# Kernel optimization log

Hardware: AMD Instinct MI355X
Metric: run time of the kernel (lower is better)

Reference implementation:

```python
import jax, jax.numpy as jnp
import numpy as np

L, N = 200, 256  # event_list_length, num_nodes


def setup_inputs() -> dict:
    key = jax.random.key(0)
    ks = jax.random.split(key, 7)
    time = jax.random.uniform(ks[0], (2,), dtype=jnp.float32)
    event_list = jax.random.normal(ks[1], (L + 1, N, N), dtype=jnp.float32)
    u_begin = jax.random.uniform(ks[2], (N, N, 3), dtype=jnp.float32)
    # xavier-ish scales for params
    a = jax.random.normal(ks[3], (L, N, N, 3), dtype=jnp.float32) * 0.05
    w = jax.random.normal(ks[4], (L, N, 1, N), dtype=jnp.float32) * 0.05
    liner_w = jax.random.normal(ks[5], (N, 3), dtype=jnp.float32) * 0.5
    liner_b = jax.random.normal(ks[6], (N,), dtype=jnp.float32) * 0.1
    return {"time": time, "event_list": event_list, "u_begin": u_begin,
            "a": a, "w": w, "liner_w": liner_w, "liner_b": liner_b,
            "batch_size": 2}


def reference(time, event_list, u_begin, a, w, liner_w, liner_b, batch_size):
    # event_list[:-1]; consumed in pairs (start, start+1) with batch_size == 2
    T = event_list.shape[0] - 1
    S = T // batch_size                      # number of scan steps
    n = event_list.shape[1]
    e2 = event_list[:T].reshape(S, 2, n, n)          # [S,2,N,N]
    a2 = a[:T].reshape(S, 2, n, n, 3)                # [S,2,N,N,3]
    w2 = w[:T, :, 0, :].reshape(S, 2, n, n)          # [S,2,N,N] (squeeze the 1-dim)
    t0, t1 = time[0], time[1]                        # original always uses time[0], time[1]

    def step(u, xs):
        ep, ap, wp = xs                              # [2,N,N], [2,N,N,3], [2,N,N]
        # per-node scalar dot: w[start][node] @ event_begin[k][node]
        dot0 = jnp.einsum('nk,nk->n', wp[0], ep[0])  # [N]
        dot1 = jnp.einsum('nk,nk->n', wp[1], ep[1])
        # math.exp in the original returns a Python float -> constant w.r.t. autograd
        f0 = jax.lax.stop_gradient(jnp.exp(-dot0 * t0))[:, None, None]
        f1 = jax.lax.stop_gradient(jnp.exp(-dot1 * t1))[:, None, None]
        lamda = u + ap[0] * f0 + ap[1] * f1          # [N,N,3]
        temp = jax.nn.softmax(lamda, axis=-1)        # softmax over the 3-dim (dim=1 of [N,3] per node)
        # per-node Linear(3,1): temp[node] @ W_node^T + b_node -> [N,N]
        out = jnp.einsum('nmc,nc->nm', temp, liner_w) + liner_b[:, None]
        # state update was .detach().cpu().numpy() -> stop_gradient
        return jax.lax.stop_gradient(temp), out

    _, outs = jax.lax.scan(step, u_begin, (e2, a2, w2))
    return outs                                      # [S, N, N] == [T/2, N, N]
```

## Files before the change

### kernel.cpp

```cpp
#include <hip/hip_runtime.h>


#define NN   256
#define TT   200
#define SS   100

__global__ __launch_bounds__(256) void fused_scan_kernel(
    const float* __restrict__ timep,
    const float* __restrict__ ev,
    const float* __restrict__ ub,
    const float* __restrict__ a,
    const float* __restrict__ w,
    const float* __restrict__ lw,
    const float* __restrict__ lb,
    float* __restrict__ out)
{
    __shared__ float fs[TT];

    const int n    = blockIdx.x;
    const int m    = threadIdx.x;
    const int lane = m & 63;
    const int wid  = m >> 6;

    const float t0 = timep[0];
    const float t1 = timep[1];
    const float tsel = (wid & 1) ? t1 : t0;

    {
        const size_t rowoff = (size_t)n * NN;
        for (int t = wid; t < TT; t += 8) {
            const int t2 = t + 4;
            const float4* wp0 = (const float4*)(w  + (size_t)t  * (NN * NN) + rowoff);
            const float4* ep0 = (const float4*)(ev + (size_t)t  * (NN * NN) + rowoff);
            const float4* wp1 = (const float4*)(w  + (size_t)t2 * (NN * NN) + rowoff);
            const float4* ep1 = (const float4*)(ev + (size_t)t2 * (NN * NN) + rowoff);
            float4 wv0 = wp0[lane];
            float4 ev0 = ep0[lane];
            float4 wv1 = wp1[lane];
            float4 ev1 = ep1[lane];
            float d0 = wv0.x * ev0.x;
            d0 = fmaf(wv0.y, ev0.y, d0);
            d0 = fmaf(wv0.z, ev0.z, d0);
            d0 = fmaf(wv0.w, ev0.w, d0);
            float d1 = wv1.x * ev1.x;
            d1 = fmaf(wv1.y, ev1.y, d1);
            d1 = fmaf(wv1.z, ev1.z, d1);
            d1 = fmaf(wv1.w, ev1.w, d1);
#pragma unroll
            for (int off = 1; off < 64; off <<= 1) {
                d0 += __shfl_xor(d0, off, 64);
                d1 += __shfl_xor(d1, off, 64);
            }
            if (lane == 0) {
                fs[t]  = __expf(-d0 * tsel);
                fs[t2] = __expf(-d1 * tsel);
            }
        }
    }
    __syncthreads();

    const size_t base    = (size_t)n * (NN * 3) + (size_t)m * 3;
    const size_t TSTRIDE = (size_t)NN * NN * 3;
    const float* ap = a + base;

    float u0 = ub[base + 0];
    float u1 = ub[base + 1];
    float u2 = ub[base + 2];

    const float w0 = lw[n * 3 + 0];
    const float w1 = lw[n * 3 + 1];
    const float w2 = lw[n * 3 + 2];
    const float bb = lb[n];

    float c0x = ap[0],            c0y = ap[1],            c0z = ap[2];
    float c1x = ap[TSTRIDE + 0],  c1y = ap[TSTRIDE + 1],  c1z = ap[TSTRIDE + 2];
    const float* ap1 = ap + 2 * TSTRIDE;
    float n0x = ap1[0],           n0y = ap1[1],           n0z = ap1[2];
    float n1x = ap1[TSTRIDE + 0], n1y = ap1[TSTRIDE + 1], n1z = ap1[TSTRIDE + 2];

    float* op = out + (size_t)n * NN + m;

    for (int s = 0; s < SS; ++s) {
        const int sp = (s + 2 < SS) ? (s + 2) : 0;
        const float* app = ap + (size_t)(2 * sp) * TSTRIDE;
        float p0x = app[0];
        float p0y = app[1];
        float p0z = app[2];
        float p1x = app[TSTRIDE + 0];
        float p1y = app[TSTRIDE + 1];
        float p1z = app[TSTRIDE + 2];

        const float f0 = fs[2 * s];
        const float f1 = fs[2 * s + 1];

        float l0 = fmaf(c0x, f0, fmaf(c1x, f1, u0));
        float l1 = fmaf(c0y, f0, fmaf(c1y, f1, u1));
        float l2 = fmaf(c0z, f0, fmaf(c1z, f1, u2));
        float mx = fmaxf(l0, fmaxf(l1, l2));
        float e0 = __expf(l0 - mx);
        float e1 = __expf(l1 - mx);
        float e2 = __expf(l2 - mx);
        float inv = __builtin_amdgcn_rcpf(e0 + e1 + e2);
        u0 = e0 * inv;
        u1 = e1 * inv;
        u2 = e2 * inv;
        op[(size_t)s * (NN * NN)] = fmaf(u0, w0, fmaf(u1, w1, fmaf(u2, w2, bb)));

        c0x = n0x; c0y = n0y; c0z = n0z;
        c1x = n1x; c1y = n1y; c1z = n1z;
        n0x = p0x; n0y = p0y; n0z = p0z;
        n1x = p1x; n1y = p1y; n1z = p1z;
    }
}

extern "C" void kernel_launch(void* const* d_in, const int* in_sizes, int n_in,
                              void* d_out, int out_size, void* d_ws, size_t ws_size,
                              hipStream_t stream) {
    const float* timep = (const float*)d_in[0];
    const float* ev    = (const float*)d_in[1];
    const float* ub    = (const float*)d_in[2];
    const float* a     = (const float*)d_in[3];
    const float* w     = (const float*)d_in[4];
    const float* lw    = (const float*)d_in[5];
    const float* lb    = (const float*)d_in[6];
    float* out = (float*)d_out;

    fused_scan_kernel<<<NN, 256, 0, stream>>>(timep, ev, ub, a, w, lw, lb, out);
}
```

Measured before the change: 305.1 us.

## Split exp-factor precompute into a wide kernel and deepen the a-prefetch pipeline

Moves the per-node dot-product and exp factor computation out of the 256-block scan kernel into its own kernel, which launches one wave per (t, n) pair and writes the results to workspace. The scan kernel then loads its 200 factors from workspace. Its prefetch of the `a` coefficients is also deepened from 2 steps ahead to 5 steps ahead, using a register ring buffer in an unrolled loop. The aim is to spread the ~100 MB of w/ev reads across many more blocks and hide more load latency in the serial scan. The cost is an extra launch, a workspace round trip, and higher register pressure.

```diff
diff --git a/kernel.cpp b/kernel.cpp
--- a/kernel.cpp
+++ b/kernel.cpp
@@ -1,62 +1,55 @@
 #include <hip/hip_runtime.h>
 
 
-#define NN   256
-#define TT   200
-#define SS   100
+#define NN 256
+#define TT 200
+#define SS 100
+#define DEPTH 5
 
-__global__ __launch_bounds__(256) void fused_scan_kernel(
+__global__ __launch_bounds__(256) void f_kernel(
     const float* __restrict__ timep,
     const float* __restrict__ ev,
+    const float* __restrict__ w,
+    float* __restrict__ fs)
+{
+    const int lane = threadIdx.x & 63;
+    const int gwave = blockIdx.x * 4 + (threadIdx.x >> 6);
+    const int t = gwave >> 8;
+    const int n = gwave & 255;
+
+    const size_t rowoff = (size_t)t * (NN * NN) + (size_t)n * NN;
+    const float4* wp = (const float4*)(w + rowoff);
+    const float4* ep = (const float4*)(ev + rowoff);
+    float4 wv = wp[lane];
+    float4 evv = ep[lane];
+    float d = wv.x * evv.x;
+    d = fmaf(wv.y, evv.y, d);
+    d = fmaf(wv.z, evv.z, d);
+    d = fmaf(wv.w, evv.w, d);
+#pragma unroll
+    for (int off = 1; off < 64; off <<= 1)
+        d += __shfl_xor(d, off, 64);
+
+    if (lane == 0) {
+        const float tsel = (t & 1) ? timep[1] : timep[0];
+        fs[n * TT + t] = __expf(-d * tsel);
+    }
+}
+
+__global__ __launch_bounds__(256) void scan_kernel(
+    const float* __restrict__ fs_g,
     const float* __restrict__ ub,
     const float* __restrict__ a,
-    const float* __restrict__ w,
     const float* __restrict__ lw,
     const float* __restrict__ lb,
     float* __restrict__ out)
 {
     __shared__ float fs[TT];
 
-    const int n    = blockIdx.x;
-    const int m    = threadIdx.x;
-    const int lane = m & 63;
-    const int wid  = m >> 6;
+    const int n = blockIdx.x;
+    const int m = threadIdx.x;
 
-    const float t0 = timep[0];
-    const float t1 = timep[1];
-    const float tsel = (wid & 1) ? t1 : t0;
-
-    {
-        const size_t rowoff = (size_t)n * NN;
-        for (int t = wid; t < TT; t += 8) {
-            const int t2 = t + 4;
-            const float4* wp0 = (const float4*)(w  + (size_t)t  * (NN * NN) + rowoff);
-            const float4* ep0 = (const float4*)(ev + (size_t)t  * (NN * NN) + rowoff);
-            const float4* wp1 = (const float4*)(w  + (size_t)t2 * (NN * NN) + rowoff);
-            const float4* ep1 = (const float4*)(ev + (size_t)t2 * (NN * NN) + rowoff);
-            float4 wv0 = wp0[lane];
-            float4 ev0 = ep0[lane];
-            float4 wv1 = wp1[lane];
-            float4 ev1 = ep1[lane];
-            float d0 = wv0.x * ev0.x;
-            d0 = fmaf(wv0.y, ev0.y, d0);
-            d0 = fmaf(wv0.z, ev0.z, d0);
-            d0 = fmaf(wv0.w, ev0.w, d0);
-            float d1 = wv1.x * ev1.x;
-            d1 = fmaf(wv1.y, ev1.y, d1);
-            d1 = fmaf(wv1.z, ev1.z, d1);
-            d1 = fmaf(wv1.w, ev1.w, d1);
-#pragma unroll
-            for (int off = 1; off < 64; off <<= 1) {
-                d0 += __shfl_xor(d0, off, 64);
-                d1 += __shfl_xor(d1, off, 64);
-            }
-            if (lane == 0) {
-                fs[t]  = __expf(-d0 * tsel);
-                fs[t2] = __expf(-d1 * tsel);
-            }
-        }
-    }
+    if (m < TT) fs[m] = fs_g[n * TT + m];
     __syncthreads();
 
     const size_t base    = (size_t)n * (NN * 3) + (size_t)m * 3;
@@ -72,44 +65,51 @@
     const float w2 = lw[n * 3 + 2];
     const float bb = lb[n];
 
-    float c0x = ap[0],            c0y = ap[1],            c0z = ap[2];
-    float c1x = ap[TSTRIDE + 0],  c1y = ap[TSTRIDE + 1],  c1z = ap[TSTRIDE + 2];
-    const float* ap1 = ap + 2 * TSTRIDE;
-    float n0x = ap1[0],           n0y = ap1[1],           n0z = ap1[2];
-    float n1x = ap1[TSTRIDE + 0], n1y = ap1[TSTRIDE + 1], n1z = ap1[TSTRIDE + 2];
-
     float* op = out + (size_t)n * NN + m;
 
-    for (int s = 0; s < SS; ++s) {
-        const int sp = (s + 2 < SS) ? (s + 2) : 0;
-        const float* app = ap + (size_t)(2 * sp) * TSTRIDE;
-        float p0x = app[0];
-        float p0y = app[1];
-        float p0z = app[2];
-        float p1x = app[TSTRIDE + 0];
-        float p1y = app[TSTRIDE + 1];
-        float p1z = app[TSTRIDE + 2];
+    float buf[DEPTH][6];
+#pragma unroll
+    for (int d = 0; d < DEPTH; ++d) {
+        const float* app = ap + (size_t)(2 * d) * TSTRIDE;
+        buf[d][0] = app[0];
+        buf[d][1] = app[1];
+        buf[d][2] = app[2];
+        buf[d][3] = app[TSTRIDE + 0];
+        buf[d][4] = app[TSTRIDE + 1];
+        buf[d][5] = app[TSTRIDE + 2];
+    }
 
-        const float f0 = fs[2 * s];
-        const float f1 = fs[2 * s + 1];
+    for (int s0 = 0; s0 < SS; s0 += DEPTH) {
+#pragma unroll
+        for (int d = 0; d < DEPTH; ++d) {
+            const int s = s0 + d;
 
-        float l0 = fmaf(c0x, f0, fmaf(c1x, f1, u0));
-        float l1 = fmaf(c0y, f0, fmaf(c1y, f1, u1));
-        float l2 = fmaf(c0z, f0, fmaf(c1z, f1, u2));
-        float mx = fmaxf(l0, fmaxf(l1, l2));
-        float e0 = __expf(l0 - mx);
-        float e1 = __expf(l1 - mx);
-        float e2 = __expf(l2 - mx);
-        float inv = __builtin_amdgcn_rcpf(e0 + e1 + e2);
-        u0 = e0 * inv;
-        u1 = e1 * inv;
-        u2 = e2 * inv;
-        op[(size_t)s * (NN * NN)] = fmaf(u0, w0, fmaf(u1, w1, fmaf(u2, w2, bb)));
+            const float f0 = fs[2 * s];
+            const float f1 = fs[2 * s + 1];
 
-        c0x = n0x; c0y = n0y; c0z = n0z;
-        c1x = n1x; c1y = n1y; c1z = n1z;
-        n0x = p0x; n0y = p0y; n0z = p0z;
-        n1x = p1x; n1y = p1y; n1z = p1z;
+            float l0 = fmaf(buf[d][0], f0, fmaf(buf[d][3], f1, u0));
+            float l1 = fmaf(buf[d][1], f0, fmaf(buf[d][4], f1, u1));
+            float l2 = fmaf(buf[d][2], f0, fmaf(buf[d][5], f1, u2));
+
+            const int sp = (s + DEPTH < SS) ? (s + DEPTH) : 0;
+            const float* app = ap + (size_t)(2 * sp) * TSTRIDE;
+            buf[d][0] = app[0];
+            buf[d][1] = app[1];
+            buf[d][2] = app[2];
+            buf[d][3] = app[TSTRIDE + 0];
+            buf[d][4] = app[TSTRIDE + 1];
+            buf[d][5] = app[TSTRIDE + 2];
+
+            float mx = fmaxf(l0, fmaxf(l1, l2));
+            float e0 = __expf(l0 - mx);
+            float e1 = __expf(l1 - mx);
+            float e2 = __expf(l2 - mx);
+            float inv = __builtin_amdgcn_rcpf(e0 + e1 + e2);
+            u0 = e0 * inv;
+            u1 = e1 * inv;
+            u2 = e2 * inv;
+            op[(size_t)s * (NN * NN)] = fmaf(u0, w0, fmaf(u1, w1, fmaf(u2, w2, bb)));
+        }
     }
 }
 
@@ -124,6 +124,8 @@
     const float* lw    = (const float*)d_in[5];
     const float* lb    = (const float*)d_in[6];
     float* out = (float*)d_out;
+    float* fs  = (float*)d_ws;
 
-    fused_scan_kernel<<<NN, 256, 0, stream>>>(timep, ev, ub, a, w, lw, lb, out);
+    f_kernel<<<(TT * NN) / 4, 256, 0, stream>>>(timep, ev, w, fs);
+    scan_kernel<<<NN, 256, 0, stream>>>(fs, ub, a, lw, lb, out);
 }
```

Result: no change. 305.7 us (+0.2%).
